# Kernel tuning notes

Measured on AMD Instinct MI355X. Metric: run time of the kernel, lower is better.

The kernel has to match this reference:

```python
import jax, jax.numpy as jnp
import numpy as np

N, L, S, E, H = 8, 4096, 4096, 256, 8
D = E // H
EPS = 1e-6


def setup_inputs() -> dict:
    key = jax.random.key(0)
    ks = jax.random.split(key, 12)
    sc = 1.0 / np.sqrt(E)
    return {
        "q": jax.random.normal(ks[0], (N, L, E), jnp.float32),
        "k": jax.random.normal(ks[1], (N, S, E), jnp.float32),
        "v": jax.random.normal(ks[2], (N, S, E), jnp.float32),
        "q_mask": jax.random.uniform(ks[3], (N, L)) > 0.2,
        "kv_mask": jax.random.uniform(ks[4], (N, S)) > 0.2,
        "Wq": jax.random.normal(ks[5], (E, E), jnp.float32) * sc,
        "bq": jax.random.normal(ks[6], (E,), jnp.float32) * sc,
        "Wk": jax.random.normal(ks[7], (E, E), jnp.float32) * sc,
        "bk": jax.random.normal(ks[8], (E,), jnp.float32) * sc,
        "Wv": jax.random.normal(ks[9], (E, E), jnp.float32) * sc,
        "bv": jax.random.normal(ks[10], (E,), jnp.float32) * sc,
        "Wm": jax.random.normal(ks[11], (E, E), jnp.float32) * sc,
    }


def reference(q, k, v, q_mask, kv_mask, Wq, bq, Wk, bk, Wv, bv, Wm):
    n, l, _ = q.shape
    s = k.shape[1]
    # QKV projections (torch Linear: x @ W.T + b), split into heads
    Q = (q @ Wq.T + bq).reshape(n, l, H, D)
    K = (k @ Wk.T + bk).reshape(n, s, H, D)
    V = (v @ Wv.T + bv).reshape(n, s, H, D)
    # elu feature map (elu(x) + 1)
    Qf = jax.nn.elu(Q) + 1.0
    Kf = jax.nn.elu(K) + 1.0
    qm = q_mask.astype(Qf.dtype)[:, :, None, None]
    km = kv_mask.astype(Kf.dtype)[:, :, None, None]
    Qf = Qf * qm
    Kf = Kf * km
    Vm = V * km / s  # values / v_length
    # KV aggregation: [n,h,d,v]
    KV = jnp.einsum('nshd,nshv->nhdv', Kf, Vm)
    # normalizer Z: [n,l,h]
    Z = 1.0 / (jnp.einsum('nlhd,nhd->nlh', Qf, Kf.sum(axis=1)) + EPS)
    out = jnp.einsum('nlhd,nhdv->nlhv', Qf, KV) * Z[..., None] * s
    # merge projection (no bias)
    return out.reshape(n, l, H * D) @ Wm.T
```

## Files before the change

### kernel.cpp

```cpp
#include <hip/hip_runtime.h>

#define EPSF 1e-6f

typedef __bf16 bf16;
typedef bf16 bf16x4 __attribute__((ext_vector_type(4)));
typedef bf16 bf16x8 __attribute__((ext_vector_type(8)));
typedef float f32x4 __attribute__((ext_vector_type(4)));
typedef unsigned int u32;


__device__ __forceinline__ void async_ld16(const void* g, void* l) {
    __builtin_amdgcn_global_load_lds(
        (const __attribute__((address_space(1))) u32*)g,
        (__attribute__((address_space(3))) u32*)l, 16, 0, 0);
}

__global__ __launch_bounds__(256) void wconv(
    const float* __restrict__ Wq, const float* __restrict__ Wk,
    const float* __restrict__ Wv, const float* __restrict__ Wm,
    bf16* __restrict__ Wb)
{
    const int b = blockIdx.x, t = threadIdx.x;
    const int m = b >> 6;
    const float* S = (m == 0) ? Wq : (m == 1) ? Wk : (m == 2) ? Wv : Wm;
    const int idx = (b & 63) * 1024 + t * 4;
    float4 v = *(const float4*)(S + idx);
    bf16x4 p = {(bf16)v.x, (bf16)v.y, (bf16)v.z, (bf16)v.w};
    *(bf16x4*)(Wb + (size_t)m * 65536 + idx) = p;
}

__global__ __launch_bounds__(256) void kvproj(
    const float* __restrict__ kin, const float* __restrict__ vin,
    const bf16* __restrict__ Wb,
    const float* __restrict__ bk, const float* __restrict__ bv,
    const int* __restrict__ kv_mask,
    float* __restrict__ KVf, float* __restrict__ Ksum)
{
    const int bx = blockIdx.x;
    const int j0 = bx * 128;
    const int n  = blockIdx.y >> 5;
    const int s0 = (blockIdx.y & 31) * 128;
    const size_t R0 = (size_t)n * 4096 + s0;

    const int t = threadIdx.x, lane = t & 63, w = t >> 6;
    const int ln15 = lane & 15, lg = lane >> 4;
    const int wm = (w >> 1) * 64, wn = (w & 1) * 64;
    const int wbase = t & ~63;

    __shared__ __align__(16) char smem[69632];
    bf16*  Kf_ld = (bf16*)smem;
    float* Xs    = (float*)(smem + 34816);
    bf16*  Ws    = (bf16*)(smem + 34816 + 16384);
    bf16*  Vm_ld = (bf16*)(smem + 34816);

    float mv[4][4];
    #pragma unroll
    for (int mi = 0; mi < 4; ++mi)
        #pragma unroll
        for (int r = 0; r < 4; ++r)
            mv[mi][r] = kv_mask[R0 + wm + mi * 16 + lg * 4 + r] ? 1.f : 0.f;

    #pragma unroll
    for (int z = 0; z < 2; ++z) {
        const float* X    = z ? vin : kin;
        const bf16*  W    = Wb + (size_t)(z + 1) * 65536;
        const float* bias = z ? bv : bk;
        bf16* Yt          = z ? Vm_ld : Kf_ld;

        f32x4 acc[4][4] = {};

        for (int k0 = 0; k0 < 256; k0 += 32) {
            #pragma unroll
            for (int i = 0; i < 4; ++i) {
                const int c = i * 256 + t, row = c >> 3, sc = c & 7;
                async_ld16(X + (R0 + row) * 256 + k0 + ((sc ^ (row & 7)) * 4),
                           Xs + (size_t)(i * 256 + wbase) * 4);
            }
            #pragma unroll
            for (int i = 0; i < 2; ++i) {
                const int c = i * 256 + t, g = c >> 3, c8 = c & 7;
                const int c8s = c8 ^ (g & 7);
                const int wrow = g * 2 + (c8s >> 2), gch = c8s & 3;
                async_ld16(W + (size_t)(j0 + wrow) * 256 + k0 + gch * 8,
                           Ws + (size_t)(i * 256 + wbase) * 8);
            }
            __syncthreads();

            bf16x8 a[4], b[4];
            #pragma unroll
            for (int mi = 0; mi < 4; ++mi) {
                const int r = wm + mi * 16 + ln15, rb = r & 7;
                f32x4 x0 = *(const f32x4*)&Xs[r * 32 + (((lg * 2)     ^ rb) * 4)];
                f32x4 x1 = *(const f32x4*)&Xs[r * 32 + (((lg * 2 + 1) ^ rb) * 4)];
                a[mi] = bf16x8{(bf16)x0[0], (bf16)x0[1], (bf16)x0[2], (bf16)x0[3],
                               (bf16)x1[0], (bf16)x1[1], (bf16)x1[2], (bf16)x1[3]};
            }
            #pragma unroll
            for (int ni = 0; ni < 4; ++ni) {
                const int wr = wn + ni * 16 + ln15, g = wr >> 1;
                const int c8 = ((wr & 1) * 4 + lg) ^ (g & 7);
                b[ni] = *(const bf16x8*)&Ws[g * 64 + c8 * 8];
            }
            #pragma unroll
            for (int mi = 0; mi < 4; ++mi)
                #pragma unroll
                for (int ni = 0; ni < 4; ++ni)
                    acc[mi][ni] = __builtin_amdgcn_mfma_f32_16x16x32_bf16(
                        a[mi], b[ni], acc[mi][ni], 0, 0, 0);
            __syncthreads();
        }

        float bb[4];
        #pragma unroll
        for (int ni = 0; ni < 4; ++ni) bb[ni] = bias[j0 + wn + ni * 16 + ln15];
        #pragma unroll
        for (int ni = 0; ni < 4; ++ni) {
            const int col = wn + ni * 16 + ln15;
            #pragma unroll
            for (int mi = 0; mi < 4; ++mi) {
                const int rowb = wm + mi * 16 + lg * 4;
                bf16x4 pk;
                #pragma unroll
                for (int r = 0; r < 4; ++r) {
                    float x = acc[mi][ni][r] + bb[ni];
                    if (z == 0) x = (x > 0.f) ? (x + 1.f) : __expf(x);
                    pk[r] = (bf16)(x * mv[mi][r]);
                }
                *(bf16x4*)&Yt[col * 136 + rowb] = pk;
            }
        }
        __syncthreads();
    }

    {
        const int c = t >> 1, sh = t & 1;
        const bf16* kp = Kf_ld + c * 136 + sh * 64;
        float s = 0.f;
        #pragma unroll
        for (int j = 0; j < 8; ++j) {
            bf16x8 vv = *(const bf16x8*)(kp + j * 8);
            #pragma unroll
            for (int jj = 0; jj < 8; ++jj) s += (float)vv[jj];
        }
        s += __shfl_xor(s, 1);
        if (sh == 0) atomicAdd(&Ksum[n * 256 + j0 + c], s);
    }

    {
        const int cb = w * 32;
        f32x4 c2[2][2] = {};
        #pragma unroll
        for (int step = 0; step < 4; ++step) {
            const int sb = step * 32 + lg * 8;
            bf16x8 a[2], b[2];
            #pragma unroll
            for (int mi = 0; mi < 2; ++mi)
                a[mi] = *(const bf16x8*)&Kf_ld[(cb + mi * 16 + ln15) * 136 + sb];
            #pragma unroll
            for (int nj = 0; nj < 2; ++nj)
                b[nj] = *(const bf16x8*)&Vm_ld[(cb + nj * 16 + ln15) * 136 + sb];
            #pragma unroll
            for (int mi = 0; mi < 2; ++mi)
                #pragma unroll
                for (int nj = 0; nj < 2; ++nj)
                    c2[mi][nj] = __builtin_amdgcn_mfma_f32_16x16x32_bf16(
                        a[mi], b[nj], c2[mi][nj], 0, 0, 0);
        }
        float* kvh = KVf + (size_t)((n * 8 + bx * 4 + w) * 1024);
        #pragma unroll
        for (int mi = 0; mi < 2; ++mi)
            #pragma unroll
            for (int nj = 0; nj < 2; ++nj)
                #pragma unroll
                for (int r = 0; r < 4; ++r)
                    atomicAdd(&kvh[(nj * 16 + ln15) * 32 + mi * 16 + lg * 4 + r],
                              c2[mi][nj][r]);
    }
}

__global__ __launch_bounds__(256) void attn(
    const float* __restrict__ qin, const bf16* __restrict__ Wb,
    const float* __restrict__ bq, const int* __restrict__ q_mask,
    const float* __restrict__ KVf, const float* __restrict__ Ksum,
    float* __restrict__ out)
{
    const int n = blockIdx.y, l0 = blockIdx.x * 64;
    const size_t R0 = (size_t)n * 4096 + l0;
    const int t = threadIdx.x, lane = t & 63, w = t >> 6;
    const int ln15 = lane & 15, lg = lane >> 4;
    const int wn = w * 64;
    const int wbase = t & ~63;

    const bf16* Wq = Wb;
    const bf16* Wm = Wb + 3 * 65536;

    __shared__ __align__(16) char smem[33792];
    float* Xs  = (float*)smem;
    bf16*  Wst = (bf16*)(smem + 8192);
    bf16 (*Qs)[264] = (bf16(*)[264])smem;
    __shared__ float KSs[256];
    __shared__ float Dens[64][9];

    KSs[t] = Ksum[n * 256 + t];

    {
        f32x4 acc[4][4] = {};
        for (int k0 = 0; k0 < 256; k0 += 32) {
            #pragma unroll
            for (int i = 0; i < 2; ++i) {
                const int c = i * 256 + t, row = c >> 3, sc = c & 7;
                async_ld16(qin + (R0 + row) * 256 + k0 + ((sc ^ (row & 7)) * 4),
                           Xs + (size_t)(i * 256 + wbase) * 4);
            }
            #pragma unroll
            for (int i = 0; i < 4; ++i) {
                const int c = i * 256 + t, g = c >> 3, c8 = c & 7;
                const int c8s = c8 ^ (g & 7);
                const int wrow = g * 2 + (c8s >> 2), gch = c8s & 3;
                async_ld16(Wq + (size_t)wrow * 256 + k0 + gch * 8,
                           Wst + (size_t)(i * 256 + wbase) * 8);
            }
            __syncthreads();

            bf16x8 a[4], b[4];
            #pragma unroll
            for (int mi = 0; mi < 4; ++mi) {
                const int r = mi * 16 + ln15, rb = r & 7;
                f32x4 x0 = *(const f32x4*)&Xs[r * 32 + (((lg * 2)     ^ rb) * 4)];
                f32x4 x1 = *(const f32x4*)&Xs[r * 32 + (((lg * 2 + 1) ^ rb) * 4)];
                a[mi] = bf16x8{(bf16)x0[0], (bf16)x0[1], (bf16)x0[2], (bf16)x0[3],
                               (bf16)x1[0], (bf16)x1[1], (bf16)x1[2], (bf16)x1[3]};
            }
            #pragma unroll
            for (int ni = 0; ni < 4; ++ni) {
                const int wr = wn + ni * 16 + ln15, g = wr >> 1;
                const int c8 = ((wr & 1) * 4 + lg) ^ (g & 7);
                b[ni] = *(const bf16x8*)&Wst[g * 64 + c8 * 8];
            }
            #pragma unroll
            for (int mi = 0; mi < 4; ++mi)
                #pragma unroll
                for (int ni = 0; ni < 4; ++ni)
                    acc[mi][ni] = __builtin_amdgcn_mfma_f32_16x16x32_bf16(
                        a[mi], b[ni], acc[mi][ni], 0, 0, 0);
            __syncthreads();
        }
        float bb[4];
        #pragma unroll
        for (int ni = 0; ni < 4; ++ni) bb[ni] = bq[wn + ni * 16 + ln15];
        float mv[4][4];
        #pragma unroll
        for (int mi = 0; mi < 4; ++mi)
            #pragma unroll
            for (int r = 0; r < 4; ++r)
                mv[mi][r] = q_mask[R0 + mi * 16 + lg * 4 + r] ? 1.f : 0.f;
        #pragma unroll
        for (int mi = 0; mi < 4; ++mi)
            #pragma unroll
            for (int r = 0; r < 4; ++r) {
                const int row = mi * 16 + lg * 4 + r;
                #pragma unroll
                for (int ni = 0; ni < 4; ++ni) {
                    float x = acc[mi][ni][r] + bb[ni];
                    x = (x > 0.f) ? (x + 1.f) : __expf(x);
                    Qs[row][wn + ni * 16 + ln15] = (bf16)(x * mv[mi][r]);
                }
            }
    }
    __syncthreads();

    #pragma unroll
    for (int i = 0; i < 2; ++i) {
        const int idx = t + i * 256;
        const int l = idx & 63, h = idx >> 6;
        float s = 0.f;
        #pragma unroll
        for (int d8 = 0; d8 < 4; ++d8) {
            bf16x8 qv = *(const bf16x8*)&Qs[l][h * 32 + d8 * 8];
            #pragma unroll
            for (int jj = 0; jj < 8; ++jj)
                s += (float)qv[jj] * KSs[h * 32 + d8 * 8 + jj];
        }
        Dens[l][h] = s;
    }
    __syncthreads();

    #pragma unroll
    for (int hh = 0; hh < 2; ++hh) {
        const int h = w * 2 + hh;
        const float* kvh = KVf + (size_t)(n * 8 + h) * 1024;
        bf16x8 a[2], b[4];
        #pragma unroll
        for (int mi = 0; mi < 2; ++mi) {
            const float* ap = kvh + (mi * 16 + ln15) * 32 + lg * 8;
            f32x4 lo = *(const f32x4*)ap;
            f32x4 hi = *(const f32x4*)(ap + 4);
            a[mi] = bf16x8{(bf16)lo[0], (bf16)lo[1], (bf16)lo[2], (bf16)lo[3],
                           (bf16)hi[0], (bf16)hi[1], (bf16)hi[2], (bf16)hi[3]};
        }
        #pragma unroll
        for (int nj = 0; nj < 4; ++nj)
            b[nj] = *(const bf16x8*)&Qs[nj * 16 + ln15][h * 32 + lg * 8];
        f32x4 c[2][4];
        #pragma unroll
        for (int mi = 0; mi < 2; ++mi)
            #pragma unroll
            for (int nj = 0; nj < 4; ++nj) {
                f32x4 zz = {};
                c[mi][nj] = __builtin_amdgcn_mfma_f32_16x16x32_bf16(a[mi], b[nj], zz, 0, 0, 0);
            }
        #pragma unroll
        for (int nj = 0; nj < 4; ++nj) {
            const int l = nj * 16 + ln15;
            const float rcp = 1.f / (Dens[l][h] + EPSF);
            #pragma unroll
            for (int mi = 0; mi < 2; ++mi) {
                bf16x4 pk;
                #pragma unroll
                for (int r = 0; r < 4; ++r) pk[r] = (bf16)(c[mi][nj][r] * rcp);
                *(bf16x4*)&Qs[l][h * 32 + mi * 16 + lg * 4] = pk;
            }
        }
    }
    __syncthreads();

    {
        f32x4 acc[4][4] = {};
        #pragma unroll 2
        for (int k0 = 0; k0 < 256; k0 += 32) {
            bf16x8 a[4], b[4];
            #pragma unroll
            for (int mi = 0; mi < 4; ++mi)
                a[mi] = *(const bf16x8*)&Qs[mi * 16 + ln15][k0 + lg * 8];
            #pragma unroll
            for (int ni = 0; ni < 4; ++ni)
                b[ni] = *(const bf16x8*)(Wm + (size_t)(wn + ni * 16 + ln15) * 256 + k0 + lg * 8);
            #pragma unroll
            for (int mi = 0; mi < 4; ++mi)
                #pragma unroll
                for (int ni = 0; ni < 4; ++ni)
                    acc[mi][ni] = __builtin_amdgcn_mfma_f32_16x16x32_bf16(
                        a[mi], b[ni], acc[mi][ni], 0, 0, 0);
        }
        #pragma unroll
        for (int ni = 0; ni < 4; ++ni) {
            const int col = wn + ni * 16 + ln15;
            #pragma unroll
            for (int mi = 0; mi < 4; ++mi)
                #pragma unroll
                for (int r = 0; r < 4; ++r)
                    out[(R0 + mi * 16 + lg * 4 + r) * 256 + col] = acc[mi][ni][r];
        }
    }
}

extern "C" void kernel_launch(void* const* d_in, const int* in_sizes, int n_in,
                              void* d_out, int out_size, void* d_ws, size_t ws_size,
                              hipStream_t stream) {
    const float* q      = (const float*)d_in[0];
    const float* k      = (const float*)d_in[1];
    const float* v      = (const float*)d_in[2];
    const int*   q_mask = (const int*)  d_in[3];
    const int*   kv_mask= (const int*)  d_in[4];
    const float* Wq     = (const float*)d_in[5];
    const float* bq     = (const float*)d_in[6];
    const float* Wk     = (const float*)d_in[7];
    const float* bk     = (const float*)d_in[8];
    const float* Wv     = (const float*)d_in[9];
    const float* bv     = (const float*)d_in[10];
    const float* Wm     = (const float*)d_in[11];

    char* ws = (char*)d_ws;
    bf16*  Wb   = (bf16*)ws;
    float* KVf  = (float*)(ws + 524288);
    float* Ksum = (float*)(ws + 524288 + 262144);

    hipMemsetAsync(ws + 524288, 0, 262144 + 8192, stream);

    const dim3 blk(256);
    wconv <<<dim3(256),    blk, 0, stream>>>(Wq, Wk, Wv, Wm, Wb);
    kvproj<<<dim3(2, 256), blk, 0, stream>>>(k, v, Wb, bk, bv, kv_mask, KVf, Ksum);
    attn  <<<dim3(64, 8),  blk, 0, stream>>>(q, Wb, bq, q_mask, KVf, Ksum, (float*)d_out);
}
```

Baseline: 203.8 us.

## Halve tile sizes and spread KV atomics across four partial slices

The KV projection kernel now processes 64-row tiles instead of 128, doubling the grid, and each block accumulates into one of four partial KV/Ksum buffers chosen by tile index to reduce atomic contention. The attention kernel uses 32-row tiles with a doubled grid and sums the four partial slices when loading KV and Ksum. This aims at better CU occupancy and less atomic serialization on MI355X. The cost is more redundant weight loading per block, a larger memset, and extra global reads to reduce the slices.

```diff
diff --git a/kernel.cpp b/kernel.cpp
--- a/kernel.cpp
+++ b/kernel.cpp
@@ -38,27 +38,29 @@
 {
     const int bx = blockIdx.x;
     const int j0 = bx * 128;
-    const int n  = blockIdx.y >> 5;
-    const int s0 = (blockIdx.y & 31) * 128;
+    const int n  = blockIdx.y >> 6;
+    const int st = blockIdx.y & 63;
+    const int s0 = st * 64;
+    const int slice = st & 3;
     const size_t R0 = (size_t)n * 4096 + s0;
 
     const int t = threadIdx.x, lane = t & 63, w = t >> 6;
     const int ln15 = lane & 15, lg = lane >> 4;
-    const int wm = (w >> 1) * 64, wn = (w & 1) * 64;
+    const int wn = w * 32;
     const int wbase = t & ~63;
 
-    __shared__ __align__(16) char smem[69632];
+    __shared__ __align__(16) char smem[36864];
     bf16*  Kf_ld = (bf16*)smem;
-    float* Xs    = (float*)(smem + 34816);
-    bf16*  Ws    = (bf16*)(smem + 34816 + 16384);
-    bf16*  Vm_ld = (bf16*)(smem + 34816);
+    float* Xs    = (float*)(smem + 18432);
+    bf16*  Ws    = (bf16*)(smem + 18432 + 8192);
+    bf16*  Vm_ld = (bf16*)(smem + 18432);
 
     float mv[4][4];
     #pragma unroll
     for (int mi = 0; mi < 4; ++mi)
         #pragma unroll
         for (int r = 0; r < 4; ++r)
-            mv[mi][r] = kv_mask[R0 + wm + mi * 16 + lg * 4 + r] ? 1.f : 0.f;
+            mv[mi][r] = kv_mask[R0 + mi * 16 + lg * 4 + r] ? 1.f : 0.f;
 
     #pragma unroll
     for (int z = 0; z < 2; ++z) {
@@ -67,11 +69,11 @@
         const float* bias = z ? bv : bk;
         bf16* Yt          = z ? Vm_ld : Kf_ld;
 
-        f32x4 acc[4][4] = {};
+        f32x4 acc[4][2] = {};
 
         for (int k0 = 0; k0 < 256; k0 += 32) {
             #pragma unroll
-            for (int i = 0; i < 4; ++i) {
+            for (int i = 0; i < 2; ++i) {
                 const int c = i * 256 + t, row = c >> 3, sc = c & 7;
                 async_ld16(X + (R0 + row) * 256 + k0 + ((sc ^ (row & 7)) * 4),
                            Xs + (size_t)(i * 256 + wbase) * 4);
@@ -86,17 +88,17 @@
             }
             __syncthreads();
 
-            bf16x8 a[4], b[4];
+            bf16x8 a[4], b[2];
             #pragma unroll
             for (int mi = 0; mi < 4; ++mi) {
-                const int r = wm + mi * 16 + ln15, rb = r & 7;
+                const int r = mi * 16 + ln15, rb = r & 7;
                 f32x4 x0 = *(const f32x4*)&Xs[r * 32 + (((lg * 2)     ^ rb) * 4)];
                 f32x4 x1 = *(const f32x4*)&Xs[r * 32 + (((lg * 2 + 1) ^ rb) * 4)];
                 a[mi] = bf16x8{(bf16)x0[0], (bf16)x0[1], (bf16)x0[2], (bf16)x0[3],
                                (bf16)x1[0], (bf16)x1[1], (bf16)x1[2], (bf16)x1[3]};
             }
             #pragma unroll
-            for (int ni = 0; ni < 4; ++ni) {
+            for (int ni = 0; ni < 2; ++ni) {
                 const int wr = wn + ni * 16 + ln15, g = wr >> 1;
                 const int c8 = ((wr & 1) * 4 + lg) ^ (g & 7);
                 b[ni] = *(const bf16x8*)&Ws[g * 64 + c8 * 8];
@@ -104,21 +106,21 @@
             #pragma unroll
             for (int mi = 0; mi < 4; ++mi)
                 #pragma unroll
-                for (int ni = 0; ni < 4; ++ni)
+                for (int ni = 0; ni < 2; ++ni)
                     acc[mi][ni] = __builtin_amdgcn_mfma_f32_16x16x32_bf16(
                         a[mi], b[ni], acc[mi][ni], 0, 0, 0);
             __syncthreads();
         }
 
-        float bb[4];
-        #pragma unroll
-        for (int ni = 0; ni < 4; ++ni) bb[ni] = bias[j0 + wn + ni * 16 + ln15];
-        #pragma unroll
-        for (int ni = 0; ni < 4; ++ni) {
+        float bb[2];
+        #pragma unroll
+        for (int ni = 0; ni < 2; ++ni) bb[ni] = bias[j0 + wn + ni * 16 + ln15];
+        #pragma unroll
+        for (int ni = 0; ni < 2; ++ni) {
             const int col = wn + ni * 16 + ln15;
             #pragma unroll
             for (int mi = 0; mi < 4; ++mi) {
-                const int rowb = wm + mi * 16 + lg * 4;
+                const int rowb = mi * 16 + lg * 4;
                 bf16x4 pk;
                 #pragma unroll
                 for (int r = 0; r < 4; ++r) {
@@ -126,7 +128,7 @@
                     if (z == 0) x = (x > 0.f) ? (x + 1.f) : __expf(x);
                     pk[r] = (bf16)(x * mv[mi][r]);
                 }
-                *(bf16x4*)&Yt[col * 136 + rowb] = pk;
+                *(bf16x4*)&Yt[col * 72 + rowb] = pk;
             }
         }
         __syncthreads();
@@ -134,31 +136,31 @@
 
     {
         const int c = t >> 1, sh = t & 1;
-        const bf16* kp = Kf_ld + c * 136 + sh * 64;
+        const bf16* kp = Kf_ld + c * 72 + sh * 32;
         float s = 0.f;
         #pragma unroll
-        for (int j = 0; j < 8; ++j) {
+        for (int j = 0; j < 4; ++j) {
             bf16x8 vv = *(const bf16x8*)(kp + j * 8);
             #pragma unroll
             for (int jj = 0; jj < 8; ++jj) s += (float)vv[jj];
         }
         s += __shfl_xor(s, 1);
-        if (sh == 0) atomicAdd(&Ksum[n * 256 + j0 + c], s);
-    }
-
-    {
-        const int cb = w * 32;
+        if (sh == 0) atomicAdd(&Ksum[slice * 2048 + n * 256 + j0 + c], s);
+    }
+
+    {
+        const int cb = wn;
         f32x4 c2[2][2] = {};
         #pragma unroll
-        for (int step = 0; step < 4; ++step) {
+        for (int step = 0; step < 2; ++step) {
             const int sb = step * 32 + lg * 8;
             bf16x8 a[2], b[2];
             #pragma unroll
             for (int mi = 0; mi < 2; ++mi)
-                a[mi] = *(const bf16x8*)&Kf_ld[(cb + mi * 16 + ln15) * 136 + sb];
+                a[mi] = *(const bf16x8*)&Kf_ld[(cb + mi * 16 + ln15) * 72 + sb];
             #pragma unroll
             for (int nj = 0; nj < 2; ++nj)
-                b[nj] = *(const bf16x8*)&Vm_ld[(cb + nj * 16 + ln15) * 136 + sb];
+                b[nj] = *(const bf16x8*)&Vm_ld[(cb + nj * 16 + ln15) * 72 + sb];
             #pragma unroll
             for (int mi = 0; mi < 2; ++mi)
                 #pragma unroll
@@ -166,7 +168,7 @@
                     c2[mi][nj] = __builtin_amdgcn_mfma_f32_16x16x32_bf16(
                         a[mi], b[nj], c2[mi][nj], 0, 0, 0);
         }
-        float* kvh = KVf + (size_t)((n * 8 + bx * 4 + w) * 1024);
+        float* kvh = KVf + (size_t)slice * 65536 + (size_t)((n * 8 + bx * 4 + w) * 1024);
         #pragma unroll
         for (int mi = 0; mi < 2; ++mi)
             #pragma unroll
@@ -184,7 +186,7 @@
     const float* __restrict__ KVf, const float* __restrict__ Ksum,
     float* __restrict__ out)
 {
-    const int n = blockIdx.y, l0 = blockIdx.x * 64;
+    const int n = blockIdx.y, l0 = blockIdx.x * 32;
     const size_t R0 = (size_t)n * 4096 + l0;
     const int t = threadIdx.x, lane = t & 63, w = t >> 6;
     const int ln15 = lane & 15, lg = lane >> 4;
@@ -194,23 +196,27 @@
     const bf16* Wq = Wb;
     const bf16* Wm = Wb + 3 * 65536;
 
-    __shared__ __align__(16) char smem[33792];
+    __shared__ __align__(16) char smem[20480];
     float* Xs  = (float*)smem;
-    bf16*  Wst = (bf16*)(smem + 8192);
+    bf16*  Wst = (bf16*)(smem + 4096);
     bf16 (*Qs)[264] = (bf16(*)[264])smem;
     __shared__ float KSs[256];
-    __shared__ float Dens[64][9];
-
-    KSs[t] = Ksum[n * 256 + t];
-
-    {
-        f32x4 acc[4][4] = {};
+    __shared__ float Dens[32][9];
+
+    {
+        float s = 0.f;
+        #pragma unroll
+        for (int sl = 0; sl < 4; ++sl) s += Ksum[sl * 2048 + n * 256 + t];
+        KSs[t] = s;
+    }
+
+    {
+        f32x4 acc[2][4] = {};
         for (int k0 = 0; k0 < 256; k0 += 32) {
-            #pragma unroll
-            for (int i = 0; i < 2; ++i) {
-                const int c = i * 256 + t, row = c >> 3, sc = c & 7;
+            {
+                const int row = t >> 3, sc = t & 7;
                 async_ld16(qin + (R0 + row) * 256 + k0 + ((sc ^ (row & 7)) * 4),
-                           Xs + (size_t)(i * 256 + wbase) * 4);
+                           Xs + (size_t)wbase * 4);
             }
             #pragma unroll
             for (int i = 0; i < 4; ++i) {
@@ -222,9 +228,9 @@
             }
             __syncthreads();
 
-            bf16x8 a[4], b[4];
-            #pragma unroll
-            for (int mi = 0; mi < 4; ++mi) {
+            bf16x8 a[2], b[4];
+            #pragma unroll
+            for (int mi = 0; mi < 2; ++mi) {
                 const int r = mi * 16 + ln15, rb = r & 7;
                 f32x4 x0 = *(const f32x4*)&Xs[r * 32 + (((lg * 2)     ^ rb) * 4)];
                 f32x4 x1 = *(const f32x4*)&Xs[r * 32 + (((lg * 2 + 1) ^ rb) * 4)];
@@ -238,7 +244,7 @@
                 b[ni] = *(const bf16x8*)&Wst[g * 64 + c8 * 8];
             }
             #pragma unroll
-            for (int mi = 0; mi < 4; ++mi)
+            for (int mi = 0; mi < 2; ++mi)
                 #pragma unroll
                 for (int ni = 0; ni < 4; ++ni)
                     acc[mi][ni] = __builtin_amdgcn_mfma_f32_16x16x32_bf16(
@@ -248,14 +254,14 @@
         float bb[4];
         #pragma unroll
         for (int ni = 0; ni < 4; ++ni) bb[ni] = bq[wn + ni * 16 + ln15];
-        float mv[4][4];
-        #pragma unroll
-        for (int mi = 0; mi < 4; ++mi)
+        float mv[2][4];
+        #pragma unroll
+        for (int mi = 0; mi < 2; ++mi)
             #pragma unroll
             for (int r = 0; r < 4; ++r)
                 mv[mi][r] = q_mask[R0 + mi * 16 + lg * 4 + r] ? 1.f : 0.f;
         #pragma unroll
-        for (int mi = 0; mi < 4; ++mi)
+        for (int mi = 0; mi < 2; ++mi)
             #pragma unroll
             for (int r = 0; r < 4; ++r) {
                 const int row = mi * 16 + lg * 4 + r;
@@ -269,10 +275,8 @@
     }
     __syncthreads();
 
-    #pragma unroll
-    for (int i = 0; i < 2; ++i) {
-        const int idx = t + i * 256;
-        const int l = idx & 63, h = idx >> 6;
+    {
+        const int l = t & 31, h = t >> 5;
         float s = 0.f;
         #pragma unroll
         for (int d8 = 0; d8 < 4; ++d8) {
@@ -288,29 +292,34 @@
     #pragma unroll
     for (int hh = 0; hh < 2; ++hh) {
         const int h = w * 2 + hh;
-        const float* kvh = KVf + (size_t)(n * 8 + h) * 1024;
-        bf16x8 a[2], b[4];
+        const size_t kvbase = (size_t)((n * 8 + h) * 1024);
+        bf16x8 a[2], b[2];
         #pragma unroll
         for (int mi = 0; mi < 2; ++mi) {
-            const float* ap = kvh + (mi * 16 + ln15) * 32 + lg * 8;
-            f32x4 lo = *(const f32x4*)ap;
-            f32x4 hi = *(const f32x4*)(ap + 4);
+            const size_t off = kvbase + (mi * 16 + ln15) * 32 + lg * 8;
+            f32x4 lo = {}, hi = {};
+            #pragma unroll
+            for (int sl = 0; sl < 4; ++sl) {
+                const float* ap = KVf + (size_t)sl * 65536 + off;
+                lo += *(const f32x4*)ap;
+                hi += *(const f32x4*)(ap + 4);
+            }
             a[mi] = bf16x8{(bf16)lo[0], (bf16)lo[1], (bf16)lo[2], (bf16)lo[3],
                            (bf16)hi[0], (bf16)hi[1], (bf16)hi[2], (bf16)hi[3]};
         }
         #pragma unroll
-        for (int nj = 0; nj < 4; ++nj)
+        for (int nj = 0; nj < 2; ++nj)
             b[nj] = *(const bf16x8*)&Qs[nj * 16 + ln15][h * 32 + lg * 8];
-        f32x4 c[2][4];
+        f32x4 c[2][2];
         #pragma unroll
         for (int mi = 0; mi < 2; ++mi)
             #pragma unroll
-            for (int nj = 0; nj < 4; ++nj) {
+            for (int nj = 0; nj < 2; ++nj) {
                 f32x4 zz = {};
                 c[mi][nj] = __builtin_amdgcn_mfma_f32_16x16x32_bf16(a[mi], b[nj], zz, 0, 0, 0);
             }
         #pragma unroll
-        for (int nj = 0; nj < 4; ++nj) {
+        for (int nj = 0; nj < 2; ++nj) {
             const int l = nj * 16 + ln15;
             const float rcp = 1.f / (Dens[l][h] + EPSF);
             #pragma unroll
@@ -325,18 +334,18 @@
     __syncthreads();
 
     {
-        f32x4 acc[4][4] = {};
+        f32x4 acc[2][4] = {};
         #pragma unroll 2
         for (int k0 = 0; k0 < 256; k0 += 32) {
-            bf16x8 a[4], b[4];
-            #pragma unroll
-            for (int mi = 0; mi < 4; ++mi)
+            bf16x8 a[2], b[4];
+            #pragma unroll
+            for (int mi = 0; mi < 2; ++mi)
                 a[mi] = *(const bf16x8*)&Qs[mi * 16 + ln15][k0 + lg * 8];
             #pragma unroll
             for (int ni = 0; ni < 4; ++ni)
                 b[ni] = *(const bf16x8*)(Wm + (size_t)(wn + ni * 16 + ln15) * 256 + k0 + lg * 8);
             #pragma unroll
-            for (int mi = 0; mi < 4; ++mi)
+            for (int mi = 0; mi < 2; ++mi)
                 #pragma unroll
                 for (int ni = 0; ni < 4; ++ni)
                     acc[mi][ni] = __builtin_amdgcn_mfma_f32_16x16x32_bf16(
@@ -346,7 +355,7 @@
         for (int ni = 0; ni < 4; ++ni) {
             const int col = wn + ni * 16 + ln15;
             #pragma unroll
-            for (int mi = 0; mi < 4; ++mi)
+            for (int mi = 0; mi < 2; ++mi)
                 #pragma unroll
                 for (int r = 0; r < 4; ++r)
                     out[(R0 + mi * 16 + lg * 4 + r) * 256 + col] = acc[mi][ni][r];
@@ -373,12 +382,12 @@
     char* ws = (char*)d_ws;
     bf16*  Wb   = (bf16*)ws;
     float* KVf  = (float*)(ws + 524288);
-    float* Ksum = (float*)(ws + 524288 + 262144);
-
-    hipMemsetAsync(ws + 524288, 0, 262144 + 8192, stream);
+    float* Ksum = (float*)(ws + 524288 + 1048576);
+
+    hipMemsetAsync(ws + 524288, 0, 1048576 + 32768, stream);
 
     const dim3 blk(256);
     wconv <<<dim3(256),    blk, 0, stream>>>(Wq, Wk, Wv, Wm, Wb);
-    kvproj<<<dim3(2, 256), blk, 0, stream>>>(k, v, Wb, bk, bv, kv_mask, KVf, Ksum);
-    attn  <<<dim3(64, 8),  blk, 0, stream>>>(q, Wb, bq, q_mask, KVf, Ksum, (float*)d_out);
-}
+    kvproj<<<dim3(2, 512), blk, 0, stream>>>(k, v, Wb, bk, bv, kv_mask, KVf, Ksum);
+    attn  <<<dim3(128, 8), blk, 0, stream>>>(q, Wb, bq, q_mask, KVf, Ksum, (float*)d_out);
+}
```

After: 257.3 us. 26.3% more time.

## Halve kvproj tile rows and replace atomics with partial buffers plus reduce kernel

Applied to the files above, without the earlier changes.

The K/V projection kernel now processes 64 sequence rows per block instead of 128, doubling the grid and halving shared memory per block. Per-block KV and Ksum partials are written with plain vector stores into a workspace buffer, replacing float atomics and the memset. A new kv_reduce kernel sums the 64 partials per (batch, head) and emits KV directly in bf16 for the attention kernel. This trades atomic contention for an extra launch and about 16 MB of partial-buffer traffic.

```diff
diff --git a/kernel.cpp b/kernel.cpp
--- a/kernel.cpp
+++ b/kernel.cpp
@@ -34,31 +34,32 @@
     const bf16* __restrict__ Wb,
     const float* __restrict__ bk, const float* __restrict__ bv,
     const int* __restrict__ kv_mask,
-    float* __restrict__ KVf, float* __restrict__ Ksum)
+    float* __restrict__ part, float* __restrict__ part_ks)
 {
     const int bx = blockIdx.x;
     const int j0 = bx * 128;
-    const int n  = blockIdx.y >> 5;
-    const int s0 = (blockIdx.y & 31) * 128;
+    const int n  = blockIdx.y >> 6;
+    const int st = blockIdx.y & 63;
+    const int s0 = st * 64;
     const size_t R0 = (size_t)n * 4096 + s0;
 
     const int t = threadIdx.x, lane = t & 63, w = t >> 6;
     const int ln15 = lane & 15, lg = lane >> 4;
-    const int wm = (w >> 1) * 64, wn = (w & 1) * 64;
+    const int wn = w * 32;
     const int wbase = t & ~63;
 
-    __shared__ __align__(16) char smem[69632];
+    __shared__ __align__(16) char smem[36864];
     bf16*  Kf_ld = (bf16*)smem;
-    float* Xs    = (float*)(smem + 34816);
-    bf16*  Ws    = (bf16*)(smem + 34816 + 16384);
-    bf16*  Vm_ld = (bf16*)(smem + 34816);
+    float* Xs    = (float*)(smem + 18432);
+    bf16*  Ws    = (bf16*)(smem + 18432 + 8192);
+    bf16*  Vm_ld = (bf16*)(smem + 18432);
 
     float mv[4][4];
     #pragma unroll
     for (int mi = 0; mi < 4; ++mi)
         #pragma unroll
         for (int r = 0; r < 4; ++r)
-            mv[mi][r] = kv_mask[R0 + wm + mi * 16 + lg * 4 + r] ? 1.f : 0.f;
+            mv[mi][r] = kv_mask[R0 + mi * 16 + lg * 4 + r] ? 1.f : 0.f;
 
     #pragma unroll
     for (int z = 0; z < 2; ++z) {
@@ -67,11 +68,11 @@
         const float* bias = z ? bv : bk;
         bf16* Yt          = z ? Vm_ld : Kf_ld;
 
-        f32x4 acc[4][4] = {};
+        f32x4 acc[4][2] = {};
 
         for (int k0 = 0; k0 < 256; k0 += 32) {
             #pragma unroll
-            for (int i = 0; i < 4; ++i) {
+            for (int i = 0; i < 2; ++i) {
                 const int c = i * 256 + t, row = c >> 3, sc = c & 7;
                 async_ld16(X + (R0 + row) * 256 + k0 + ((sc ^ (row & 7)) * 4),
                            Xs + (size_t)(i * 256 + wbase) * 4);
@@ -86,17 +87,17 @@
             }
             __syncthreads();
 
-            bf16x8 a[4], b[4];
+            bf16x8 a[4], b[2];
             #pragma unroll
             for (int mi = 0; mi < 4; ++mi) {
-                const int r = wm + mi * 16 + ln15, rb = r & 7;
+                const int r = mi * 16 + ln15, rb = r & 7;
                 f32x4 x0 = *(const f32x4*)&Xs[r * 32 + (((lg * 2)     ^ rb) * 4)];
                 f32x4 x1 = *(const f32x4*)&Xs[r * 32 + (((lg * 2 + 1) ^ rb) * 4)];
                 a[mi] = bf16x8{(bf16)x0[0], (bf16)x0[1], (bf16)x0[2], (bf16)x0[3],
                                (bf16)x1[0], (bf16)x1[1], (bf16)x1[2], (bf16)x1[3]};
             }
             #pragma unroll
-            for (int ni = 0; ni < 4; ++ni) {
+            for (int ni = 0; ni < 2; ++ni) {
                 const int wr = wn + ni * 16 + ln15, g = wr >> 1;
                 const int c8 = ((wr & 1) * 4 + lg) ^ (g & 7);
                 b[ni] = *(const bf16x8*)&Ws[g * 64 + c8 * 8];
@@ -104,21 +105,21 @@
             #pragma unroll
             for (int mi = 0; mi < 4; ++mi)
                 #pragma unroll
-                for (int ni = 0; ni < 4; ++ni)
+                for (int ni = 0; ni < 2; ++ni)
                     acc[mi][ni] = __builtin_amdgcn_mfma_f32_16x16x32_bf16(
                         a[mi], b[ni], acc[mi][ni], 0, 0, 0);
             __syncthreads();
         }
 
-        float bb[4];
-        #pragma unroll
-        for (int ni = 0; ni < 4; ++ni) bb[ni] = bias[j0 + wn + ni * 16 + ln15];
-        #pragma unroll
-        for (int ni = 0; ni < 4; ++ni) {
+        float bb[2];
+        #pragma unroll
+        for (int ni = 0; ni < 2; ++ni) bb[ni] = bias[j0 + wn + ni * 16 + ln15];
+        #pragma unroll
+        for (int ni = 0; ni < 2; ++ni) {
             const int col = wn + ni * 16 + ln15;
             #pragma unroll
             for (int mi = 0; mi < 4; ++mi) {
-                const int rowb = wm + mi * 16 + lg * 4;
+                const int rowb = mi * 16 + lg * 4;
                 bf16x4 pk;
                 #pragma unroll
                 for (int r = 0; r < 4; ++r) {
@@ -126,7 +127,7 @@
                     if (z == 0) x = (x > 0.f) ? (x + 1.f) : __expf(x);
                     pk[r] = (bf16)(x * mv[mi][r]);
                 }
-                *(bf16x4*)&Yt[col * 136 + rowb] = pk;
+                *(bf16x4*)&Yt[col * 72 + rowb] = pk;
             }
         }
         __syncthreads();
@@ -134,31 +135,31 @@
 
     {
         const int c = t >> 1, sh = t & 1;
-        const bf16* kp = Kf_ld + c * 136 + sh * 64;
+        const bf16* kp = Kf_ld + c * 72 + sh * 32;
         float s = 0.f;
         #pragma unroll
-        for (int j = 0; j < 8; ++j) {
+        for (int j = 0; j < 4; ++j) {
             bf16x8 vv = *(const bf16x8*)(kp + j * 8);
             #pragma unroll
             for (int jj = 0; jj < 8; ++jj) s += (float)vv[jj];
         }
         s += __shfl_xor(s, 1);
-        if (sh == 0) atomicAdd(&Ksum[n * 256 + j0 + c], s);
+        if (sh == 0) part_ks[((size_t)(n * 64 + st)) * 256 + j0 + c] = s;
     }
 
     {
-        const int cb = w * 32;
+        const int cb = wn;
         f32x4 c2[2][2] = {};
         #pragma unroll
-        for (int step = 0; step < 4; ++step) {
+        for (int step = 0; step < 2; ++step) {
             const int sb = step * 32 + lg * 8;
             bf16x8 a[2], b[2];
             #pragma unroll
             for (int mi = 0; mi < 2; ++mi)
-                a[mi] = *(const bf16x8*)&Kf_ld[(cb + mi * 16 + ln15) * 136 + sb];
+                a[mi] = *(const bf16x8*)&Kf_ld[(cb + mi * 16 + ln15) * 72 + sb];
             #pragma unroll
             for (int nj = 0; nj < 2; ++nj)
-                b[nj] = *(const bf16x8*)&Vm_ld[(cb + nj * 16 + ln15) * 136 + sb];
+                b[nj] = *(const bf16x8*)&Vm_ld[(cb + nj * 16 + ln15) * 72 + sb];
             #pragma unroll
             for (int mi = 0; mi < 2; ++mi)
                 #pragma unroll
@@ -166,22 +167,39 @@
                     c2[mi][nj] = __builtin_amdgcn_mfma_f32_16x16x32_bf16(
                         a[mi], b[nj], c2[mi][nj], 0, 0, 0);
         }
-        float* kvh = KVf + (size_t)((n * 8 + bx * 4 + w) * 1024);
+        float* kvh = part + ((size_t)((n * 64 + st) * 8) + bx * 4 + w) * 1024;
         #pragma unroll
         for (int mi = 0; mi < 2; ++mi)
             #pragma unroll
             for (int nj = 0; nj < 2; ++nj)
-                #pragma unroll
-                for (int r = 0; r < 4; ++r)
-                    atomicAdd(&kvh[(nj * 16 + ln15) * 32 + mi * 16 + lg * 4 + r],
-                              c2[mi][nj][r]);
+                *(f32x4*)&kvh[(nj * 16 + ln15) * 32 + mi * 16 + lg * 4] = c2[mi][nj];
+    }
+}
+
+__global__ __launch_bounds__(256) void kv_reduce(
+    const float* __restrict__ part, const float* __restrict__ part_ks,
+    bf16* __restrict__ KVb, float* __restrict__ Ksum)
+{
+    const int nh = blockIdx.x, n = nh >> 3, h = nh & 7;
+    const int t = threadIdx.x;
+    f32x4 acc = {};
+    const float* p = part + ((size_t)n * 512 + h) * 1024 + t * 4;
+    for (int c = 0; c < 64; ++c)
+        acc += *(const f32x4*)(p + (size_t)c * 8192);
+    bf16x4 ob = {(bf16)acc[0], (bf16)acc[1], (bf16)acc[2], (bf16)acc[3]};
+    *(bf16x4*)(KVb + (size_t)nh * 1024 + t * 4) = ob;
+    if (t < 32) {
+        float s = 0.f;
+        const float* pk = part_ks + (size_t)n * 16384 + h * 32 + t;
+        for (int c = 0; c < 64; ++c) s += pk[c * 256];
+        Ksum[n * 256 + h * 32 + t] = s;
     }
 }
 
 __global__ __launch_bounds__(256) void attn(
     const float* __restrict__ qin, const bf16* __restrict__ Wb,
     const float* __restrict__ bq, const int* __restrict__ q_mask,
-    const float* __restrict__ KVf, const float* __restrict__ Ksum,
+    const bf16* __restrict__ KVb, const float* __restrict__ Ksum,
     float* __restrict__ out)
 {
     const int n = blockIdx.y, l0 = blockIdx.x * 64;
@@ -288,16 +306,11 @@
     #pragma unroll
     for (int hh = 0; hh < 2; ++hh) {
         const int h = w * 2 + hh;
-        const float* kvh = KVf + (size_t)(n * 8 + h) * 1024;
+        const bf16* kvh = KVb + (size_t)(n * 8 + h) * 1024;
         bf16x8 a[2], b[4];
         #pragma unroll
-        for (int mi = 0; mi < 2; ++mi) {
-            const float* ap = kvh + (mi * 16 + ln15) * 32 + lg * 8;
-            f32x4 lo = *(const f32x4*)ap;
-            f32x4 hi = *(const f32x4*)(ap + 4);
-            a[mi] = bf16x8{(bf16)lo[0], (bf16)lo[1], (bf16)lo[2], (bf16)lo[3],
-                           (bf16)hi[0], (bf16)hi[1], (bf16)hi[2], (bf16)hi[3]};
-        }
+        for (int mi = 0; mi < 2; ++mi)
+            a[mi] = *(const bf16x8*)(kvh + (mi * 16 + ln15) * 32 + lg * 8);
         #pragma unroll
         for (int nj = 0; nj < 4; ++nj)
             b[nj] = *(const bf16x8*)&Qs[nj * 16 + ln15][h * 32 + lg * 8];
@@ -371,14 +384,15 @@
     const float* Wm     = (const float*)d_in[11];
 
     char* ws = (char*)d_ws;
-    bf16*  Wb   = (bf16*)ws;
-    float* KVf  = (float*)(ws + 524288);
-    float* Ksum = (float*)(ws + 524288 + 262144);
-
-    hipMemsetAsync(ws + 524288, 0, 262144 + 8192, stream);
+    bf16*  Wb      = (bf16*)ws;
+    float* part    = (float*)(ws + 524288);
+    float* part_ks = (float*)(ws + 524288 + 16777216);
+    bf16*  KVb     = (bf16*)(ws + 524288 + 16777216 + 524288);
+    float* Ksum    = (float*)(ws + 524288 + 16777216 + 524288 + 131072);
 
     const dim3 blk(256);
-    wconv <<<dim3(256),    blk, 0, stream>>>(Wq, Wk, Wv, Wm, Wb);
-    kvproj<<<dim3(2, 256), blk, 0, stream>>>(k, v, Wb, bk, bv, kv_mask, KVf, Ksum);
-    attn  <<<dim3(64, 8),  blk, 0, stream>>>(q, Wb, bq, q_mask, KVf, Ksum, (float*)d_out);
-}
+    wconv    <<<dim3(256),    blk, 0, stream>>>(Wq, Wk, Wv, Wm, Wb);
+    kvproj   <<<dim3(2, 512), blk, 0, stream>>>(k, v, Wb, bk, bv, kv_mask, part, part_ks);
+    kv_reduce<<<dim3(64),     blk, 0, stream>>>(part, part_ks, KVb, Ksum);
+    attn     <<<dim3(64, 8),  blk, 0, stream>>>(q, Wb, bq, q_mask, KVb, Ksum, (float*)d_out);
+}
```

After: 199.2 us. 2.3% less time.
